# Kernel optimization log

Measured on AMD Instinct MI355X. Metric: run time of the kernel, lower is better.

## Reference

```python
import jax, jax.numpy as jnp
import numpy as np


def _xavier(key, shape):
    fan_out, fan_in = shape
    lim = float(np.sqrt(6.0 / (fan_in + fan_out)))
    return jax.random.uniform(key, shape, jnp.float32, -lim, lim)


def setup_inputs() -> dict:
    B, I, H, P = 8192, 1024, 1024, 2048
    key = jax.random.key(0)
    ks = jax.random.split(key, 12)
    return {
        "x": jax.random.normal(ks[0], (B, I), jnp.float32),
        "hidden": jax.random.normal(ks[1], (B, H), jnp.float32),
        "persistent_memory": jax.random.normal(ks[2], (B, P), jnp.float32),
        # attention_gate: Linear(H,H), 'gate' bias init = -0.1
        "Wa": _xavier(ks[3], (H, H)), "ba": jnp.full((H,), -0.1, jnp.float32),
        # reset/update/new gates: Linear(I+H, H), 'gate' bias init = -0.1
        "Wr": _xavier(ks[4], (H, I + H)), "br": jnp.full((H,), -0.1, jnp.float32),
        "Wu": _xavier(ks[5], (H, I + H)), "bu": jnp.full((H,), -0.1, jnp.float32),
        "Wn": _xavier(ks[6], (H, I + H)), "bn": jnp.full((H,), -0.1, jnp.float32),
        # memory read/write/address: Linear(H,P), zero bias; forget bias = 1.0
        "Wread": _xavier(ks[7], (P, H)), "bread": jnp.zeros((P,), jnp.float32),
        "Wwrite": _xavier(ks[8], (P, H)), "bwrite": jnp.zeros((P,), jnp.float32),
        "Wforget": _xavier(ks[9], (P, H)), "bforget": jnp.ones((P,), jnp.float32),
        "Waddr": _xavier(ks[10], (P, H)), "baddr": jnp.zeros((P,), jnp.float32),
        "connection_strength": jnp.ones((H,), jnp.float32),
        "connection_decay": jnp.full((1,), 0.99, jnp.float32),
        "connection_history": jnp.zeros((H,), jnp.float32),  # buffer, starts at 0
    }


def reference(x, hidden, persistent_memory, Wa, ba, Wr, br, Wu, bu, Wn, bn,
              Wread, bread, Wwrite, bwrite, Wforget, bforget, Waddr, baddr,
              connection_strength, connection_decay, connection_history):
    H = hidden.shape[1]
    # update_connections (reward=None): history*decay + detached mean(|h|) over batch
    activity = jax.lax.stop_gradient(jnp.mean(jnp.abs(hidden), axis=0))  # [H]
    ch = connection_history * connection_decay + activity
    cs = connection_strength * jax.nn.sigmoid(ch)  # [H]

    attention = jax.nn.sigmoid(hidden @ Wa.T + ba)
    ha = hidden * attention
    combined = jnp.concatenate([x, ha], axis=1)
    reset = combined @ Wr.T + br
    update = combined @ Wu.T + bu
    combined_reset = jnp.concatenate([x, reset * ha], axis=1)
    new = combined_reset @ Wn.T + bn
    # neuromodulators=None: apply_neuromodulation returns gates UNACTIVATED (faithful)
    hidden_new = (1.0 - update) * hidden + update * new * cs[None, :]  # [B,H]

    addr = jax.nn.softmax(hidden_new @ Waddr.T + baddr, axis=1)        # [B,P]
    read = jax.nn.sigmoid(hidden_new @ Wread.T + bread)
    write = jax.nn.sigmoid(hidden_new @ Wwrite.T + bwrite)
    forget = jax.nn.sigmoid(hidden_new @ Wforget.T + bforget)

    # F.linear with ones(P,H)/H weight == row-mean of hidden_new broadcast to P
    hp = jnp.mean(hidden_new, axis=1, keepdims=True)                   # [B,1]
    memory_new = forget * persistent_memory + write * hp * addr        # [B,P]
    memory_read_content = read * memory_new
    # F.linear with ones(H,P)/P weight == row-mean over P broadcast to H
    hidden_final = hidden_new + jnp.mean(memory_read_content, axis=1, keepdims=True)
    return hidden_final, memory_new
```

## Files before the change

kernel.cpp:

```cpp
#include <hip/hip_runtime.h>

typedef unsigned short u16;
typedef short bfrag __attribute__((ext_vector_type(8)));
typedef float f32x4 __attribute__((ext_vector_type(4)));
typedef const __attribute__((address_space(1))) unsigned int* gp1_t;
typedef __attribute__((address_space(3))) unsigned int* lp3_t;

#define B_ 8192
#define H_ 1024
#define P_ 2048

__device__ __forceinline__ u16 f2bf(float f) {
  unsigned u = __builtin_bit_cast(unsigned, f);
  u += 0x7fffu + ((u >> 16) & 1u);
  return (u16)(u >> 16);
}
__device__ __forceinline__ float bf2f(u16 s) {
  return __builtin_bit_cast(float, (unsigned)s << 16);
}
__device__ __forceinline__ float sigm(float v) { return 1.f / (1.f + __expf(-v)); }


__global__ void k_activity(const float* __restrict__ hidden, float* __restrict__ act) {
  int t = threadIdx.x;
  const float* p = hidden + (size_t)blockIdx.x * 128 * H_;
  float s0 = 0, s1 = 0, s2 = 0, s3 = 0;
  for (int r = 0; r < 128; ++r) {
    const float* q = p + (size_t)r * H_;
    s0 += fabsf(q[t]); s1 += fabsf(q[t + 256]);
    s2 += fabsf(q[t + 512]); s3 += fabsf(q[t + 768]);
  }
  atomicAdd(&act[t], s0); atomicAdd(&act[t + 256], s1);
  atomicAdd(&act[t + 512], s2); atomicAdd(&act[t + 768], s3);
}

__global__ void k_cs(const float* __restrict__ act, const float* __restrict__ strength,
                     const float* __restrict__ decay, const float* __restrict__ hist,
                     float* __restrict__ cs) {
  int h = blockIdx.x * 256 + threadIdx.x;
  float ch = hist[h] * decay[0] + act[h] * (1.f / (float)B_);
  cs[h] = strength[h] * sigm(ch);
}

__global__ void k_f32_to_bf16(const float* __restrict__ s, u16* __restrict__ d, int n4) {
  int i = blockIdx.x * blockDim.x + threadIdx.x;
  if (i < n4) {
    float4 v = ((const float4*)s)[i];
    ushort4 o;
    o.x = f2bf(v.x); o.y = f2bf(v.y); o.z = f2bf(v.z); o.w = f2bf(v.w);
    ((ushort4*)d)[i] = o;
  }
}

__global__ void k_pack_x(const float* __restrict__ x, u16* __restrict__ comb) {
  int i = blockIdx.x * blockDim.x + threadIdx.x;
  int row = i >> 8;
  int c4 = i & 255;
  float4 v = ((const float4*)x)[i];
  ushort4 o;
  o.x = f2bf(v.x); o.y = f2bf(v.y); o.z = f2bf(v.z); o.w = f2bf(v.w);
  *(ushort4*)&comb[(size_t)row * 2048 + c4 * 4] = o;
}

__global__ void k_creset(const float* __restrict__ reset, u16* __restrict__ comb) {
  int i = blockIdx.x * blockDim.x + threadIdx.x;
  int row = i >> 8;
  int c4 = i & 255;
  float4 r = ((const float4*)reset)[i];
  u16* p = &comb[(size_t)row * 2048 + 1024 + c4 * 4];
  ushort4 h = *(ushort4*)p;
  ushort4 o;
  o.x = f2bf(r.x * bf2f(h.x)); o.y = f2bf(r.y * bf2f(h.y));
  o.z = f2bf(r.z * bf2f(h.z)); o.w = f2bf(r.w * bf2f(h.w));
  *(ushort4*)p = o;
}

__global__ void k_rowmean(const float* __restrict__ hn, float* __restrict__ hp) {
  int row = blockIdx.x * 4 + (threadIdx.x >> 6);
  int lane = threadIdx.x & 63;
  const float* p = hn + (size_t)row * H_;
  float s = 0.f;
#pragma unroll
  for (int c = 0; c < H_ / 64; ++c) s += p[lane + c * 64];
#pragma unroll
  for (int o = 32; o; o >>= 1) s += __shfl_down(s, o);
  if (lane == 0) hp[row] = s * (1.f / (float)H_);
}


struct GemmPs {
  const u16* Bm[4];
  const float* bias[4];
  const float* hidden;
  const float* update;
  const float* cs;
  float* out_f0;
  float* out_f1;
  float* hn_f32;
  u16* hn_bf16;
  u16* combined;
  u16* out_b[4];
};

template <int EPI>
__device__ __forceinline__ void epi(int row, int col, float v, int z, const GemmPs& e) {
  if constexpr (EPI == 1) {
    v += e.bias[0][col];
    float a = sigm(v);
    float ha = e.hidden[(size_t)row * H_ + col] * a;
    e.combined[(size_t)row * 2048 + 1024 + col] = f2bf(ha);
  } else if constexpr (EPI == 2) {
    v += e.bias[z][col];
    float* o = (z == 0) ? e.out_f0 : e.out_f1;
    o[(size_t)row * H_ + col] = v;
  } else if constexpr (EPI == 3) {
    v += e.bias[0][col];
    size_t i = (size_t)row * H_ + col;
    float u = e.update[i];
    float hn = (1.f - u) * e.hidden[i] + u * v * e.cs[col];
    e.hn_f32[i] = hn;
    e.hn_bf16[i] = f2bf(hn);
  } else {
    v += e.bias[z][col];
    e.out_b[z][(size_t)row * P_ + col] = f2bf(v);
  }
}

template <int EPI>
__global__ __launch_bounds__(256, 2) void gemm_bt(const u16* __restrict__ A, int K, GemmPs e) {
  const int z = blockIdx.z;
  const u16* __restrict__ Bm = e.Bm[z];
  __shared__ u16 As[128 * 64];
  __shared__ u16 Bs[128 * 64];
  const int lane = threadIdx.x & 63;
  const int w = threadIdx.x >> 6;
  const int wr = w >> 1, wc = w & 1;
  const int m0 = blockIdx.x * 128, n0 = blockIdx.y * 128;

  f32x4 acc[4][4] = {};

  const int rA = lane >> 3;
  const int srcSlot = (lane & 7) ^ (rA & 7);
  const u16* pA = A + (size_t)(m0 + w * 32 + rA) * K + srcSlot * 8;
  const u16* pB = Bm + (size_t)(n0 + w * 32 + rA) * K + srcSlot * 8;

  const int g = lane >> 4;
  const int r15 = lane & 15;
  const int rx = lane & 7;

  for (int k0 = 0; k0 < K; k0 += 64) {
#pragma unroll
    for (int j = 0; j < 4; ++j) {
      __builtin_amdgcn_global_load_lds((gp1_t)(pA + (size_t)j * 8 * K + k0),
                                       (lp3_t)&As[(w * 32 + j * 8) * 64], 16, 0, 0);
      __builtin_amdgcn_global_load_lds((gp1_t)(pB + (size_t)j * 8 * K + k0),
                                       (lp3_t)&Bs[(w * 32 + j * 8) * 64], 16, 0, 0);
    }
    asm volatile("s_waitcnt vmcnt(0)" ::: "memory");
    __syncthreads();
#pragma unroll
    for (int kk = 0; kk < 64; kk += 32) {
      const int slot = g + (kk >> 3);
      const int cswz = ((slot ^ rx) << 3);
      bfrag af[4], bq[4];
#pragma unroll
      for (int i = 0; i < 4; ++i) {
        af[i] = *(const bfrag*)&As[(wr * 64 + i * 16 + r15) * 64 + cswz];
        bq[i] = *(const bfrag*)&Bs[(wc * 64 + i * 16 + r15) * 64 + cswz];
      }
#pragma unroll
      for (int mi = 0; mi < 4; ++mi)
#pragma unroll
        for (int ni = 0; ni < 4; ++ni)
          acc[mi][ni] = __builtin_amdgcn_mfma_f32_16x16x32_bf16(af[mi], bq[ni], acc[mi][ni], 0, 0, 0);
    }
    __syncthreads();
  }

#pragma unroll
  for (int mi = 0; mi < 4; ++mi)
#pragma unroll
    for (int ni = 0; ni < 4; ++ni)
#pragma unroll
      for (int r = 0; r < 4; ++r)
        epi<EPI>(m0 + wr * 64 + mi * 16 + g * 4 + r,
                 n0 + wc * 64 + ni * 16 + r15, acc[mi][ni][r], z, e);
}


__global__ __launch_bounds__(256) void k_final(
    const u16* __restrict__ aL, const u16* __restrict__ rL,
    const u16* __restrict__ wL, const u16* __restrict__ fL,
    const float* __restrict__ pm, const float* __restrict__ hn,
    const float* __restrict__ hp, float* __restrict__ outH, float* __restrict__ outM) {
  __shared__ float sl[P_];
  __shared__ float red[8];
  const int row = blockIdx.x, t = threadIdx.x;
  const size_t base = (size_t)row * P_;

  float lm = -3.4e38f;
  for (int p = t; p < P_; p += 256) {
    float v = bf2f(aL[base + p]);
    sl[p] = v;
    lm = fmaxf(lm, v);
  }
#pragma unroll
  for (int o = 32; o; o >>= 1) lm = fmaxf(lm, __shfl_down(lm, o));
  if ((t & 63) == 0) red[t >> 6] = lm;
  __syncthreads();
  const float bmax = fmaxf(fmaxf(red[0], red[1]), fmaxf(red[2], red[3]));

  float ls = 0.f;
  for (int p = t; p < P_; p += 256) {
    float ev = __expf(sl[p] - bmax);
    sl[p] = ev;
    ls += ev;
  }
#pragma unroll
  for (int o = 32; o; o >>= 1) ls += __shfl_down(ls, o);
  if ((t & 63) == 0) red[4 + (t >> 6)] = ls;
  __syncthreads();
  const float inv = 1.f / (red[4] + red[5] + red[6] + red[7]);
  const float hpv = hp[row];

  float rs = 0.f;
  for (int p = t; p < P_; p += 256) {
    float a = sl[p] * inv;
    float fo = sigm(bf2f(fL[base + p]));
    float wv = sigm(bf2f(wL[base + p]));
    float rd = sigm(bf2f(rL[base + p]));
    float mem = fo * pm[base + p] + wv * hpv * a;
    outM[base + p] = mem;
    rs += rd * mem;
  }
#pragma unroll
  for (int o = 32; o; o >>= 1) rs += __shfl_down(rs, o);
  __syncthreads();
  if ((t & 63) == 0) red[t >> 6] = rs;
  __syncthreads();
  const float mean = (red[0] + red[1] + red[2] + red[3]) * (1.f / (float)P_);
  const size_t hb = (size_t)row * H_;
  for (int h = t; h < H_; h += 256) outH[hb + h] = hn[hb + h] + mean;
}


extern "C" void kernel_launch(void* const* d_in, const int* in_sizes, int n_in,
                              void* d_out, int out_size, void* d_ws, size_t ws_size,
                              hipStream_t stream) {
  (void)in_sizes; (void)n_in; (void)out_size; (void)ws_size;
  const float* x       = (const float*)d_in[0];
  const float* hidden  = (const float*)d_in[1];
  const float* pm      = (const float*)d_in[2];
  const float* Wa      = (const float*)d_in[3];
  const float* ba      = (const float*)d_in[4];
  const float* Wr      = (const float*)d_in[5];
  const float* br      = (const float*)d_in[6];
  const float* Wu      = (const float*)d_in[7];
  const float* bu      = (const float*)d_in[8];
  const float* Wn      = (const float*)d_in[9];
  const float* bn      = (const float*)d_in[10];
  const float* Wread   = (const float*)d_in[11];
  const float* bread   = (const float*)d_in[12];
  const float* Wwrite  = (const float*)d_in[13];
  const float* bwrite  = (const float*)d_in[14];
  const float* Wforget = (const float*)d_in[15];
  const float* bforget = (const float*)d_in[16];
  const float* Waddr   = (const float*)d_in[17];
  const float* baddr   = (const float*)d_in[18];
  const float* cstr    = (const float*)d_in[19];
  const float* cdecay  = (const float*)d_in[20];
  const float* chist   = (const float*)d_in[21];

  char* wsp = (char*)d_ws;
  auto take = [&](size_t n) { char* p = wsp; wsp += (n + 255) & ~(size_t)255; return p; };
  float* act    = (float*)take((size_t)H_ * 4);
  float* cs     = (float*)take((size_t)H_ * 4);
  float* hp     = (float*)take((size_t)B_ * 4);
  u16* hiddenB  = (u16*)take((size_t)B_ * H_ * 2);
  u16* WaB      = (u16*)take((size_t)H_ * H_ * 2);
  u16* WrB      = (u16*)take((size_t)H_ * 2048 * 2);
  u16* WuB      = (u16*)take((size_t)H_ * 2048 * 2);
  u16* WnB      = (u16*)take((size_t)H_ * 2048 * 2);
  u16* WadB     = (u16*)take((size_t)P_ * H_ * 2);
  u16* WrdB     = (u16*)take((size_t)P_ * H_ * 2);
  u16* WwrB     = (u16*)take((size_t)P_ * H_ * 2);
  u16* WfgB     = (u16*)take((size_t)P_ * H_ * 2);
  u16* combined = (u16*)take((size_t)B_ * 2048 * 2);
  float* reset  = (float*)take((size_t)B_ * H_ * 4);
  float* update = (float*)take((size_t)B_ * H_ * 4);
  float* hnf    = (float*)take((size_t)B_ * H_ * 4);
  u16* gAd      = (u16*)take((size_t)B_ * P_ * 2);
  u16* gRd      = (u16*)take((size_t)B_ * P_ * 2);
  u16* gWr      = (u16*)take((size_t)B_ * P_ * 2);
  u16* gFg      = (u16*)take((size_t)B_ * P_ * 2);

  float* outH = (float*)d_out;
  float* outM = outH + (size_t)B_ * H_;

  hipMemsetAsync(act, 0, (size_t)H_ * 4, stream);
  k_activity<<<dim3(64), dim3(256), 0, stream>>>(hidden, act);
  k_cs<<<dim3(4), dim3(256), 0, stream>>>(act, cstr, cdecay, chist, cs);

  auto conv = [&](const float* s, u16* d, size_t n) {
    k_f32_to_bf16<<<dim3((unsigned)(n / 4 / 256)), dim3(256), 0, stream>>>(s, d, (int)(n / 4));
  };
  conv(Wa, WaB, (size_t)H_ * H_);
  conv(Wr, WrB, (size_t)H_ * 2048);
  conv(Wu, WuB, (size_t)H_ * 2048);
  conv(Wn, WnB, (size_t)H_ * 2048);
  conv(Waddr, WadB, (size_t)P_ * H_);
  conv(Wread, WrdB, (size_t)P_ * H_);
  conv(Wwrite, WwrB, (size_t)P_ * H_);
  conv(Wforget, WfgB, (size_t)P_ * H_);
  conv(hidden, hiddenB, (size_t)B_ * H_);
  k_pack_x<<<dim3(8192), dim3(256), 0, stream>>>(x, combined);

  {
    GemmPs e{};
    e.Bm[0] = WaB; e.bias[0] = ba; e.hidden = hidden; e.combined = combined;
    gemm_bt<1><<<dim3(64, 8, 1), dim3(256), 0, stream>>>(hiddenB, 1024, e);
  }
  {
    GemmPs e{};
    e.Bm[0] = WrB; e.Bm[1] = WuB; e.bias[0] = br; e.bias[1] = bu;
    e.out_f0 = reset; e.out_f1 = update;
    gemm_bt<2><<<dim3(64, 8, 2), dim3(256), 0, stream>>>(combined, 2048, e);
  }
  k_creset<<<dim3(8192), dim3(256), 0, stream>>>(reset, combined);
  {
    GemmPs e{};
    e.Bm[0] = WnB; e.bias[0] = bn; e.hidden = hidden; e.update = update; e.cs = cs;
    e.hn_f32 = hnf; e.hn_bf16 = hiddenB;
    gemm_bt<3><<<dim3(64, 8, 1), dim3(256), 0, stream>>>(combined, 2048, e);
  }
  k_rowmean<<<dim3(2048), dim3(256), 0, stream>>>(hnf, hp);
  {
    GemmPs e{};
    e.Bm[0] = WadB; e.Bm[1] = WrdB; e.Bm[2] = WwrB; e.Bm[3] = WfgB;
    e.bias[0] = baddr; e.bias[1] = bread; e.bias[2] = bwrite; e.bias[3] = bforget;
    e.out_b[0] = gAd; e.out_b[1] = gRd; e.out_b[2] = gWr; e.out_b[3] = gFg;
    gemm_bt<4><<<dim3(64, 16, 4), dim3(256), 0, stream>>>(hiddenB, 1024, e);
  }
  k_final<<<dim3(B_), dim3(256), 0, stream>>>(gAd, gRd, gWr, gFg, pm, hnf, hp, outH, outM);
}
```

Baseline: 462.6 us.

## Replace GEMM with 256x256 double-buffered 8-wave kernel and fuse elementwise passes

Replaces the 128x128 single-buffer GEMM with a 512-thread, 256x256-tile kernel. It double-buffers LDS with direct global-to-LDS loads, interleaves MFMA quadrants with barriers and priority raising, and remaps block order for L2 locality. Concatenated inputs become two separate A pointers split at K0, which drops the combined buffer and the pack step. The reset*ha product moves into the reset GEMM epilogue, removing the fp32 reset buffer and the k_creset pass. Weight conversions merge into one multi-tensor launch, and the hidden bf16 cast fuses with the activity reduction. The larger tiles use more LDS and registers and reduce the number of blocks, which may lower occupancy.

```diff
diff --git a/kernel.cpp b/kernel.cpp
--- a/kernel.cpp
+++ b/kernel.cpp
@@ -21,17 +21,26 @@
 __device__ __forceinline__ float sigm(float v) { return 1.f / (1.f + __expf(-v)); }
 
 
-__global__ void k_activity(const float* __restrict__ hidden, float* __restrict__ act) {
-  int t = threadIdx.x;
-  const float* p = hidden + (size_t)blockIdx.x * 128 * H_;
-  float s0 = 0, s1 = 0, s2 = 0, s3 = 0;
-  for (int r = 0; r < 128; ++r) {
-    const float* q = p + (size_t)r * H_;
-    s0 += fabsf(q[t]); s1 += fabsf(q[t + 256]);
-    s2 += fabsf(q[t + 512]); s3 += fabsf(q[t + 768]);
-  }
-  atomicAdd(&act[t], s0); atomicAdd(&act[t + 256], s1);
-  atomicAdd(&act[t + 512], s2); atomicAdd(&act[t + 768], s3);
+__global__ void k_hidact(const float* __restrict__ hidden, u16* __restrict__ hB,
+                         float* __restrict__ act) {
+  const int t = threadIdx.x;
+  const int r0 = blockIdx.x * 16;
+  float s00 = 0, s01 = 0, s10 = 0, s11 = 0;
+  for (int r = 0; r < 16; ++r) {
+    const float* q = hidden + (size_t)(r0 + r) * H_;
+    u16* o = hB + (size_t)(r0 + r) * H_;
+    float2 v0 = *(const float2*)&q[2 * t];
+    float2 v1 = *(const float2*)&q[512 + 2 * t];
+    s00 += fabsf(v0.x); s01 += fabsf(v0.y);
+    s10 += fabsf(v1.x); s11 += fabsf(v1.y);
+    ushort2 o0, o1;
+    o0.x = f2bf(v0.x); o0.y = f2bf(v0.y);
+    o1.x = f2bf(v1.x); o1.y = f2bf(v1.y);
+    *(ushort2*)&o[2 * t] = o0;
+    *(ushort2*)&o[512 + 2 * t] = o1;
+  }
+  atomicAdd(&act[2 * t], s00); atomicAdd(&act[2 * t + 1], s01);
+  atomicAdd(&act[512 + 2 * t], s10); atomicAdd(&act[512 + 2 * t + 1], s11);
 }
 
 __global__ void k_cs(const float* __restrict__ act, const float* __restrict__ strength,
@@ -42,37 +51,23 @@
   cs[h] = strength[h] * sigm(ch);
 }
 
-__global__ void k_f32_to_bf16(const float* __restrict__ s, u16* __restrict__ d, int n4) {
-  int i = blockIdx.x * blockDim.x + threadIdx.x;
-  if (i < n4) {
-    float4 v = ((const float4*)s)[i];
+struct ConvPs {
+  const float* s[9];
+  u16* d[9];
+  int n4[9];
+};
+
+__global__ void k_conv9(ConvPs p) {
+  const int e = blockIdx.y;
+  const int n4 = p.n4[e];
+  const float4* s = (const float4*)p.s[e];
+  ushort4* d = (ushort4*)p.d[e];
+  for (int i = blockIdx.x * 256 + threadIdx.x; i < n4; i += 2048 * 256) {
+    float4 v = s[i];
     ushort4 o;
     o.x = f2bf(v.x); o.y = f2bf(v.y); o.z = f2bf(v.z); o.w = f2bf(v.w);
-    ((ushort4*)d)[i] = o;
-  }
-}
-
-__global__ void k_pack_x(const float* __restrict__ x, u16* __restrict__ comb) {
-  int i = blockIdx.x * blockDim.x + threadIdx.x;
-  int row = i >> 8;
-  int c4 = i & 255;
-  float4 v = ((const float4*)x)[i];
-  ushort4 o;
-  o.x = f2bf(v.x); o.y = f2bf(v.y); o.z = f2bf(v.z); o.w = f2bf(v.w);
-  *(ushort4*)&comb[(size_t)row * 2048 + c4 * 4] = o;
-}
-
-__global__ void k_creset(const float* __restrict__ reset, u16* __restrict__ comb) {
-  int i = blockIdx.x * blockDim.x + threadIdx.x;
-  int row = i >> 8;
-  int c4 = i & 255;
-  float4 r = ((const float4*)reset)[i];
-  u16* p = &comb[(size_t)row * 2048 + 1024 + c4 * 4];
-  ushort4 h = *(ushort4*)p;
-  ushort4 o;
-  o.x = f2bf(r.x * bf2f(h.x)); o.y = f2bf(r.y * bf2f(h.y));
-  o.z = f2bf(r.z * bf2f(h.z)); o.w = f2bf(r.w * bf2f(h.w));
-  *(ushort4*)p = o;
+    d[i] = o;
+  }
 }
 
 __global__ void k_rowmean(const float* __restrict__ hn, float* __restrict__ hp) {
@@ -94,11 +89,12 @@
   const float* hidden;
   const float* update;
   const float* cs;
-  float* out_f0;
+  const u16* haB;
+  u16* rhaB;
   float* out_f1;
   float* hn_f32;
   u16* hn_bf16;
-  u16* combined;
+  u16* haB_out;
   u16* out_b[4];
 };
 
@@ -107,12 +103,17 @@
   if constexpr (EPI == 1) {
     v += e.bias[0][col];
     float a = sigm(v);
-    float ha = e.hidden[(size_t)row * H_ + col] * a;
-    e.combined[(size_t)row * 2048 + 1024 + col] = f2bf(ha);
+    size_t i = (size_t)row * H_ + col;
+    e.haB_out[i] = f2bf(e.hidden[i] * a);
   } else if constexpr (EPI == 2) {
-    v += e.bias[z][col];
-    float* o = (z == 0) ? e.out_f0 : e.out_f1;
-    o[(size_t)row * H_ + col] = v;
+    size_t i = (size_t)row * H_ + col;
+    if (z == 0) {
+      v += e.bias[0][col];
+      e.rhaB[i] = f2bf(v * bf2f(e.haB[i]));
+    } else {
+      v += e.bias[1][col];
+      e.out_f1[i] = v;
+    }
   } else if constexpr (EPI == 3) {
     v += e.bias[0][col];
     size_t i = (size_t)row * H_ + col;
@@ -126,65 +127,138 @@
   }
 }
 
+#define QUAD(Af, Bf, MO, NO)                                                         \
+  do {                                                                               \
+    _Pragma("unroll") for (int ks = 0; ks < 2; ++ks)                                 \
+    _Pragma("unroll") for (int mi = 0; mi < 4; ++mi)                                 \
+    _Pragma("unroll") for (int ni = 0; ni < 2; ++ni)                                 \
+      acc[(MO) + mi][(NO) + ni] = __builtin_amdgcn_mfma_f32_16x16x32_bf16(           \
+          Af[mi][ks], Bf[ni][ks], acc[(MO) + mi][(NO) + ni], 0, 0, 0);               \
+  } while (0)
+
+#define LGKM0()                                           \
+  do {                                                    \
+    asm volatile("s_waitcnt lgkmcnt(0)" ::: "memory");    \
+    __builtin_amdgcn_sched_barrier(0);                    \
+  } while (0)
+
 template <int EPI>
-__global__ __launch_bounds__(256, 2) void gemm_bt(const u16* __restrict__ A, int K, GemmPs e) {
+__global__ __launch_bounds__(512, 2) void gemm8(const u16* __restrict__ A0,
+                                                const u16* __restrict__ A1,
+                                                int K0, int K, GemmPs e) {
+  __shared__ u16 As[2][256 * 64];
+  __shared__ u16 Bs[2][256 * 64];
   const int z = blockIdx.z;
-  const u16* __restrict__ Bm = e.Bm[z];
-  __shared__ u16 As[128 * 64];
-  __shared__ u16 Bs[128 * 64];
-  const int lane = threadIdx.x & 63;
-  const int w = threadIdx.x >> 6;
-  const int wr = w >> 1, wc = w & 1;
-  const int m0 = blockIdx.x * 128, n0 = blockIdx.y * 128;
-
-  f32x4 acc[4][4] = {};
-
-  const int rA = lane >> 3;
-  const int srcSlot = (lane & 7) ^ (rA & 7);
-  const u16* pA = A + (size_t)(m0 + w * 32 + rA) * K + srcSlot * 8;
-  const u16* pB = Bm + (size_t)(n0 + w * 32 + rA) * K + srcSlot * 8;
-
-  const int g = lane >> 4;
-  const int r15 = lane & 15;
-  const int rx = lane & 7;
-
-  for (int k0 = 0; k0 < K; k0 += 64) {
-#pragma unroll
-    for (int j = 0; j < 4; ++j) {
-      __builtin_amdgcn_global_load_lds((gp1_t)(pA + (size_t)j * 8 * K + k0),
-                                       (lp3_t)&As[(w * 32 + j * 8) * 64], 16, 0, 0);
-      __builtin_amdgcn_global_load_lds((gp1_t)(pB + (size_t)j * 8 * K + k0),
-                                       (lp3_t)&Bs[(w * 32 + j * 8) * 64], 16, 0, 0);
+  const u16* __restrict__ Bw = e.Bm[z];
+
+  int bid = blockIdx.x;
+  const int cpx = gridDim.x >> 3;
+  bid = (bid & 7) * cpx + (bid >> 3);
+  const int m0 = (bid & 31) << 8;
+  const int n0 = (bid >> 5) << 8;
+
+  const int tid = threadIdx.x;
+  const int lane = tid & 63;
+  const int w = tid >> 6;
+  const int wr = w >> 2, wc = w & 3;
+  const int r15 = lane & 15, g = lane >> 4, rx = lane & 7;
+
+  const int srow = tid >> 3;
+  const int sslot8 = ((tid & 7) ^ (srow & 7)) << 3;
+
+  f32x4 acc[8][4] = {};
+
+  auto stage = [&](int buf, int kt) {
+    const int k0 = kt << 6;
+    const u16* Ab; int sA, kl;
+    if (k0 < K0) { Ab = A0; sA = K0; kl = k0; }
+    else         { Ab = A1; sA = K - K0; kl = k0 - K0; }
+    const u16* pa = Ab + (size_t)(m0 + srow) * sA + kl + sslot8;
+    const u16* pb = Bw + (size_t)(n0 + srow) * K + k0 + sslot8;
+    u16* la = &As[buf][(w * 8) * 64];
+    u16* lb = &Bs[buf][(w * 8) * 64];
+#pragma unroll
+    for (int r = 0; r < 4; ++r) {
+      __builtin_amdgcn_global_load_lds((gp1_t)(pa + (size_t)(r * 64) * sA),
+                                       (lp3_t)(la + r * 64 * 64), 16, 0, 0);
+      __builtin_amdgcn_global_load_lds((gp1_t)(pb + (size_t)(r * 64) * K),
+                                       (lp3_t)(lb + r * 64 * 64), 16, 0, 0);
     }
-    asm volatile("s_waitcnt vmcnt(0)" ::: "memory");
-    __syncthreads();
-#pragma unroll
-    for (int kk = 0; kk < 64; kk += 32) {
-      const int slot = g + (kk >> 3);
-      const int cswz = ((slot ^ rx) << 3);
-      bfrag af[4], bq[4];
-#pragma unroll
-      for (int i = 0; i < 4; ++i) {
-        af[i] = *(const bfrag*)&As[(wr * 64 + i * 16 + r15) * 64 + cswz];
-        bq[i] = *(const bfrag*)&Bs[(wc * 64 + i * 16 + r15) * 64 + cswz];
-      }
-#pragma unroll
-      for (int mi = 0; mi < 4; ++mi)
-#pragma unroll
-        for (int ni = 0; ni < 4; ++ni)
-          acc[mi][ni] = __builtin_amdgcn_mfma_f32_16x16x32_bf16(af[mi], bq[ni], acc[mi][ni], 0, 0, 0);
+  };
+
+  const int nt = K >> 6;
+  stage(0, 0);
+  stage(1, 1);
+  asm volatile("s_waitcnt vmcnt(8)" ::: "memory");
+  __builtin_amdgcn_s_barrier();
+
+  bfrag af[4][2], b0[2][2], b1[2][2];
+
+  for (int t = 0; t < nt; ++t) {
+    const int buf = t & 1;
+#pragma unroll
+    for (int mi = 0; mi < 4; ++mi)
+#pragma unroll
+      for (int ks = 0; ks < 2; ++ks)
+        af[mi][ks] = *(const bfrag*)&As[buf][(wr * 128 + mi * 16 + r15) * 64 +
+                                            (((g + ks * 4) ^ rx) << 3)];
+#pragma unroll
+    for (int ni = 0; ni < 2; ++ni)
+#pragma unroll
+      for (int ks = 0; ks < 2; ++ks)
+        b0[ni][ks] = *(const bfrag*)&Bs[buf][(wc * 64 + ni * 16 + r15) * 64 +
+                                            (((g + ks * 4) ^ rx) << 3)];
+    __builtin_amdgcn_s_barrier();
+    LGKM0();
+    __builtin_amdgcn_s_setprio(1);
+    QUAD(af, b0, 0, 0);
+    __builtin_amdgcn_s_setprio(0);
+    __builtin_amdgcn_s_barrier();
+#pragma unroll
+    for (int ni = 0; ni < 2; ++ni)
+#pragma unroll
+      for (int ks = 0; ks < 2; ++ks)
+        b1[ni][ks] = *(const bfrag*)&Bs[buf][(wc * 64 + 32 + ni * 16 + r15) * 64 +
+                                            (((g + ks * 4) ^ rx) << 3)];
+    __builtin_amdgcn_s_barrier();
+    LGKM0();
+    __builtin_amdgcn_s_setprio(1);
+    QUAD(af, b1, 0, 2);
+    __builtin_amdgcn_s_setprio(0);
+    __builtin_amdgcn_s_barrier();
+#pragma unroll
+    for (int mi = 0; mi < 4; ++mi)
+#pragma unroll
+      for (int ks = 0; ks < 2; ++ks)
+        af[mi][ks] = *(const bfrag*)&As[buf][(wr * 128 + 64 + mi * 16 + r15) * 64 +
+                                            (((g + ks * 4) ^ rx) << 3)];
+    __builtin_amdgcn_s_barrier();
+    LGKM0();
+    __builtin_amdgcn_s_setprio(1);
+    QUAD(af, b0, 4, 0);
+    __builtin_amdgcn_s_setprio(0);
+    __builtin_amdgcn_s_barrier();
+    if (t + 2 < nt) {
+      stage(buf, t + 2);
+      asm volatile("s_waitcnt vmcnt(8)" ::: "memory");
+    } else {
+      asm volatile("s_waitcnt vmcnt(0)" ::: "memory");
     }
-    __syncthreads();
-  }
-
-#pragma unroll
-  for (int mi = 0; mi < 4; ++mi)
+    __builtin_amdgcn_s_barrier();
+    __builtin_amdgcn_s_setprio(1);
+    QUAD(af, b1, 4, 2);
+    __builtin_amdgcn_s_setprio(0);
+    __builtin_amdgcn_s_barrier();
+  }
+
+#pragma unroll
+  for (int mi = 0; mi < 8; ++mi)
 #pragma unroll
     for (int ni = 0; ni < 4; ++ni)
 #pragma unroll
-      for (int r = 0; r < 4; ++r)
-        epi<EPI>(m0 + wr * 64 + mi * 16 + g * 4 + r,
-                 n0 + wc * 64 + ni * 16 + r15, acc[mi][ni][r], z, e);
+      for (int rr = 0; rr < 4; ++rr)
+        epi<EPI>(m0 + wr * 128 + mi * 16 + g * 4 + rr,
+                 n0 + wc * 64 + ni * 16 + r15, acc[mi][ni][rr], z, e);
 }
 
 
@@ -277,6 +351,9 @@
   float* cs     = (float*)take((size_t)H_ * 4);
   float* hp     = (float*)take((size_t)B_ * 4);
   u16* hiddenB  = (u16*)take((size_t)B_ * H_ * 2);
+  u16* xB       = (u16*)take((size_t)B_ * H_ * 2);
+  u16* haB      = (u16*)take((size_t)B_ * H_ * 2);
+  u16* rhaB     = (u16*)take((size_t)B_ * H_ * 2);
   u16* WaB      = (u16*)take((size_t)H_ * H_ * 2);
   u16* WrB      = (u16*)take((size_t)H_ * 2048 * 2);
   u16* WuB      = (u16*)take((size_t)H_ * 2048 * 2);
@@ -285,8 +362,6 @@
   u16* WrdB     = (u16*)take((size_t)P_ * H_ * 2);
   u16* WwrB     = (u16*)take((size_t)P_ * H_ * 2);
   u16* WfgB     = (u16*)take((size_t)P_ * H_ * 2);
-  u16* combined = (u16*)take((size_t)B_ * 2048 * 2);
-  float* reset  = (float*)take((size_t)B_ * H_ * 4);
   float* update = (float*)take((size_t)B_ * H_ * 4);
   float* hnf    = (float*)take((size_t)B_ * H_ * 4);
   u16* gAd      = (u16*)take((size_t)B_ * P_ * 2);
@@ -298,40 +373,35 @@
   float* outM = outH + (size_t)B_ * H_;
 
   hipMemsetAsync(act, 0, (size_t)H_ * 4, stream);
-  k_activity<<<dim3(64), dim3(256), 0, stream>>>(hidden, act);
+  k_hidact<<<dim3(512), dim3(256), 0, stream>>>(hidden, hiddenB, act);
   k_cs<<<dim3(4), dim3(256), 0, stream>>>(act, cstr, cdecay, chist, cs);
 
-  auto conv = [&](const float* s, u16* d, size_t n) {
-    k_f32_to_bf16<<<dim3((unsigned)(n / 4 / 256)), dim3(256), 0, stream>>>(s, d, (int)(n / 4));
-  };
-  conv(Wa, WaB, (size_t)H_ * H_);
-  conv(Wr, WrB, (size_t)H_ * 2048);
-  conv(Wu, WuB, (size_t)H_ * 2048);
-  conv(Wn, WnB, (size_t)H_ * 2048);
-  conv(Waddr, WadB, (size_t)P_ * H_);
-  conv(Wread, WrdB, (size_t)P_ * H_);
-  conv(Wwrite, WwrB, (size_t)P_ * H_);
-  conv(Wforget, WfgB, (size_t)P_ * H_);
-  conv(hidden, hiddenB, (size_t)B_ * H_);
-  k_pack_x<<<dim3(8192), dim3(256), 0, stream>>>(x, combined);
+  {
+    ConvPs p;
+    const float* ss[9] = {Wa, Wr, Wu, Wn, Waddr, Wread, Wwrite, Wforget, x};
+    u16* dd[9] = {WaB, WrB, WuB, WnB, WadB, WrdB, WwrB, WfgB, xB};
+    int nn[9] = {H_ * H_ / 4, H_ * 2048 / 4, H_ * 2048 / 4, H_ * 2048 / 4,
+                 P_ * H_ / 4, P_ * H_ / 4, P_ * H_ / 4, P_ * H_ / 4, B_ * H_ / 4};
+    for (int i = 0; i < 9; ++i) { p.s[i] = ss[i]; p.d[i] = dd[i]; p.n4[i] = nn[i]; }
+    k_conv9<<<dim3(2048, 9), dim3(256), 0, stream>>>(p);
+  }
 
   {
     GemmPs e{};
-    e.Bm[0] = WaB; e.bias[0] = ba; e.hidden = hidden; e.combined = combined;
-    gemm_bt<1><<<dim3(64, 8, 1), dim3(256), 0, stream>>>(hiddenB, 1024, e);
+    e.Bm[0] = WaB; e.bias[0] = ba; e.hidden = hidden; e.haB_out = haB;
+    gemm8<1><<<dim3(128, 1, 1), dim3(512), 0, stream>>>(hiddenB, hiddenB, 1024, 1024, e);
   }
   {
     GemmPs e{};
     e.Bm[0] = WrB; e.Bm[1] = WuB; e.bias[0] = br; e.bias[1] = bu;
-    e.out_f0 = reset; e.out_f1 = update;
-    gemm_bt<2><<<dim3(64, 8, 2), dim3(256), 0, stream>>>(combined, 2048, e);
-  }
-  k_creset<<<dim3(8192), dim3(256), 0, stream>>>(reset, combined);
+    e.haB = haB; e.rhaB = rhaB; e.out_f1 = update;
+    gemm8<2><<<dim3(128, 1, 2), dim3(512), 0, stream>>>(xB, haB, 1024, 2048, e);
+  }
   {
     GemmPs e{};
     e.Bm[0] = WnB; e.bias[0] = bn; e.hidden = hidden; e.update = update; e.cs = cs;
     e.hn_f32 = hnf; e.hn_bf16 = hiddenB;
-    gemm_bt<3><<<dim3(64, 8, 1), dim3(256), 0, stream>>>(combined, 2048, e);
+    gemm8<3><<<dim3(128, 1, 1), dim3(512), 0, stream>>>(xB, rhaB, 1024, 2048, e);
   }
   k_rowmean<<<dim3(2048), dim3(256), 0, stream>>>(hnf, hp);
   {
@@ -339,7 +409,7 @@
     e.Bm[0] = WadB; e.Bm[1] = WrdB; e.Bm[2] = WwrB; e.Bm[3] = WfgB;
     e.bias[0] = baddr; e.bias[1] = bread; e.bias[2] = bwrite; e.bias[3] = bforget;
     e.out_b[0] = gAd; e.out_b[1] = gRd; e.out_b[2] = gWr; e.out_b[3] = gFg;
-    gemm_bt<4><<<dim3(64, 16, 4), dim3(256), 0, stream>>>(hiddenB, 1024, e);
+    gemm8<4><<<dim3(256, 1, 4), dim3(512), 0, stream>>>(hiddenB, hiddenB, 1024, 1024, e);
   }
   k_final<<<dim3(B_), dim3(256), 0, stream>>>(gAd, gRd, gWr, gFg, pm, hnf, hp, outH, outM);
 }
```

Result: slower. 588.9 us (+27.3%).
